# Performance work log

Measured on AMD Instinct MI355X. Metric: run time of the kernel, lower is better.

## Reference

```python
import jax, jax.numpy as jnp
import numpy as np

BLK = 128          # stk blocking
HID = 1024         # hidden_size
FFN = 4096         # ffn_hidden_size per expert
NE = 8             # moe_num_experts
TOK = 8192         # padded tokens (multiple of BLK)


def setup_inputs() -> dict:
    key = jax.random.key(0)
    k1, k2, k3 = jax.random.split(key, 3)
    x = jax.random.normal(k1, (TOK, HID), dtype=jnp.float32)
    w1 = jax.random.normal(k2, (NE * FFN, HID), dtype=jnp.float32) * 0.02
    n_row_blocks = TOK // BLK          # 64
    cols_per_expert = FFN // BLK       # 32
    # dMoE topology: each token row-block is assigned one expert; its nonzero
    # column blocks are all ffn blocks of that expert.
    expert_assign = jax.random.randint(k3, (n_row_blocks,), 0, NE)
    row_indices = jnp.repeat(jnp.arange(n_row_blocks), cols_per_expert)
    column_indices = (expert_assign[:, None] * cols_per_expert
                      + jnp.arange(cols_per_expert)[None, :]).reshape(-1)
    return {
        "x": x,
        "w1": w1,
        "row_indices": row_indices.astype(jnp.int32),     # [nnz]
        "column_indices": column_indices.astype(jnp.int32),  # [nnz]
        "block": BLK,
    }


def reference(x, w1, row_indices, column_indices, block):
    # sdd(x, w1.T, topo): out block k = x_block[row_indices[k]] @ w1_block[column_indices[k]].T
    hid = x.shape[1]
    xb = x.reshape(-1, block, hid)    # [n_row_blocks, blk, hid]
    wb = w1.reshape(-1, block, hid)   # [n_col_blocks, blk, hid]
    # [nnz, blk, blk] block-sparse data of the output matrix
    return jnp.einsum('kbh,kch->kbc', xb[row_indices], wb[column_indices])
```

## Files before the change

kernel.cpp:

```cpp
#include <hip/hip_runtime.h>
#include <hip/hip_bf16.h>
#include <stdint.h>

#define HID 1024
#define BLKDIM 128
#define BKT 32
#define NKT (HID / BKT)
#define NBUF 3

using short8 = __attribute__((ext_vector_type(8))) short;
using f32x4  = __attribute__((ext_vector_type(4))) float;
using f32x4v = __attribute__((ext_vector_type(4))) float;

__device__ __forceinline__ uint32_t bfround(float f) {
    uint32_t u = __builtin_bit_cast(uint32_t, f);
    return (u + 0x7FFFu + ((u >> 16) & 1u)) >> 16;
}

__device__ __forceinline__ void gld16(const ushort* g, const ushort* lds_base) {
    __builtin_amdgcn_global_load_lds(
        (const __attribute__((address_space(1))) void*)g,
        (__attribute__((address_space(3))) void*)lds_base, 16, 0, 0);
}

__global__ __launch_bounds__(256)
void cvt_sched_kernel(const float* __restrict__ x, const float* __restrict__ w1,
                      uint4* __restrict__ xb, uint4* __restrict__ wb,
                      int nx8, int nw8,
                      const int* __restrict__ cind, int* __restrict__ perm) {
    const int t = threadIdx.x;
    if (blockIdx.x == 0) {
        __shared__ int er[64], srb[64], goff[9];
        if (t < 64) er[t] = (cind[t * 32] >> 5) & 7;
        __syncthreads();
        if (t == 0) {
            int cnt[8], off[8];
            for (int e = 0; e < 8; ++e) cnt[e] = 0;
            for (int r = 0; r < 64; ++r) cnt[er[r]]++;
            goff[0] = 0;
            for (int e = 0; e < 8; ++e) { goff[e + 1] = goff[e] + cnt[e]; off[e] = goff[e]; }
            for (int r = 0; r < 64; ++r) srb[off[er[r]]++] = r;
        }
        __syncthreads();
        for (int g = t; g < 1024; g += 256) {
            int e = 0;
            while (g >= goff[e + 1] * 16) ++e;
            const int ne = goff[e + 1] - goff[e];
            const int local = g - goff[e] * 16;
            const int j = local / ne;
            const int idx = local - j * ne;
            perm[g] = srb[goff[e] + idx] * 16 + j;
        }
    }
    const int i = blockIdx.x * 256 + t;
    if (i < nx8) {
        const f32x4v* s = reinterpret_cast<const f32x4v*>(x) + (size_t)i * 2;
        f32x4v v0 = __builtin_nontemporal_load(s);
        f32x4v v1 = __builtin_nontemporal_load(s + 1);
        uint4 w;
        w.x = bfround(v0.x) | (bfround(v0.y) << 16);
        w.y = bfround(v0.z) | (bfround(v0.w) << 16);
        w.z = bfround(v1.x) | (bfround(v1.y) << 16);
        w.w = bfround(v1.z) | (bfround(v1.w) << 16);
        xb[i] = w;
    } else if (i < nx8 + nw8) {
        const int j = i - nx8;
        const f32x4v* s = reinterpret_cast<const f32x4v*>(w1) + (size_t)j * 2;
        f32x4v v0 = __builtin_nontemporal_load(s);
        f32x4v v1 = __builtin_nontemporal_load(s + 1);
        uint4 w;
        w.x = bfround(v0.x) | (bfround(v0.y) << 16);
        w.y = bfround(v0.z) | (bfround(v0.w) << 16);
        w.z = bfround(v1.x) | (bfround(v1.y) << 16);
        w.w = bfround(v1.z) | (bfround(v1.w) << 16);
        wb[j] = w;
    }
}

__global__ __launch_bounds__(512, 4)
void sdd_pipe2_kernel(const ushort* __restrict__ xb, const ushort* __restrict__ wb,
                      const int* __restrict__ rind, const int* __restrict__ cind,
                      const int* __restrict__ perm,
                      float* __restrict__ out) {
    __shared__ ushort lds[NBUF * BLKDIM * BKT + NBUF * 2 * BLKDIM * BKT];

    int g = blockIdx.x;
    const int nwg = gridDim.x;
    if ((nwg & 7) == 0) {
        const int cpx = nwg >> 3;
        g = (g & 7) * cpx + (g >> 3);
    }
    g = perm[g];
    const int k0 = g * 2;
    const int r  = rind[k0];

    const int t = threadIdx.x;
    const int w = t >> 6;
    const int l = t & 63;

    ushort* sAb = lds;
    ushort* sBb = lds + NBUF * BLKDIM * BKT;

    const int unx   = (l & 7) ^ ((l >> 3) & 7);
    const int rin16 = 2 * (l >> 3) + (unx >> 2);
    const int kofs  = (unx & 3) * 8;

    const ushort* agb = xb + (size_t)(r * BLKDIM + w * 16 + rin16) * HID + kofs;
    const int cblk = cind[k0 + (w >> 2)];
    const ushort* bgb = wb + (size_t)(cblk * BLKDIM + (w & 3) * 32 + rin16) * HID + kofs;

    const int wr   = (w >> 2) * 64;
    const int wcol = (w & 3) * 64;
    const int ps_l = (((l >> 4) + ((l & 1) << 2)) ^ ((l & 15) >> 1)) * 8;
    const int rhalf = (l & 15) >> 1;

    int aoff[4], boff[4];
#pragma unroll
    for (int m = 0; m < 4; ++m) aoff[m] = (wr / 2 + m * 8 + rhalf) * 64 + ps_l;
#pragma unroll
    for (int n = 0; n < 4; ++n) boff[n] = (wcol / 2 + n * 8 + rhalf) * 64 + ps_l;

    f32x4 acc[4][4];
#pragma unroll
    for (int m = 0; m < 4; ++m)
#pragma unroll
        for (int n = 0; n < 4; ++n)
            acc[m][n] = (f32x4){0.f, 0.f, 0.f, 0.f};

    auto stage = [&](int b, int kt) {
        gld16(agb + kt * BKT, &sAb[b * 4096 + w * 512]);
        gld16(bgb + kt * BKT,                      &sBb[b * 8192 + (2 * w) * 512]);
        gld16(bgb + (size_t)16 * HID + kt * BKT,   &sBb[b * 8192 + (2 * w + 1) * 512]);
    };

    stage(0, 0);
    stage(1, 1);
    asm volatile("s_waitcnt vmcnt(3)" ::: "memory");
    __builtin_amdgcn_s_barrier();
    __builtin_amdgcn_sched_barrier(0);

    for (int kt = 0; kt < NKT; ++kt) {
        const int cur = kt % 3;
        const int nxt = (kt + 2) % 3;
        const bool pre = (kt + 2) < NKT;
        const ushort* sa = &sAb[cur * 4096];
        const ushort* sb = &sBb[cur * 8192];

        short8 aF[4], bF[4];
#pragma unroll
        for (int m = 0; m < 4; ++m)
            aF[m] = *reinterpret_cast<const short8*>(&sa[aoff[m]]);
#pragma unroll
        for (int n = 0; n < 4; ++n)
            bF[n] = *reinterpret_cast<const short8*>(&sb[boff[n]]);
        if (pre) stage(nxt, kt + 2);
        __builtin_amdgcn_s_setprio(1);
#pragma unroll
        for (int m = 0; m < 4; ++m)
#pragma unroll
            for (int n = 0; n < 4; ++n)
                acc[m][n] = __builtin_amdgcn_mfma_f32_16x16x32_bf16(aF[m], bF[n], acc[m][n], 0, 0, 0);
        __builtin_amdgcn_s_setprio(0);

        if (pre) asm volatile("s_waitcnt vmcnt(3)" ::: "memory");
        else     asm volatile("s_waitcnt vmcnt(0)" ::: "memory");
        __builtin_amdgcn_s_barrier();
        __builtin_amdgcn_sched_barrier(0);
    }

    const int blk = (w & 3) >> 1;
    float* op = out + (size_t)(k0 + blk) * (BLKDIM * BLKDIM);
    const int colbase = (wcol & 64) ? 64 : 0;
    float* scr = reinterpret_cast<float*>(lds) + w * 1216;

#pragma unroll
    for (int m = 0; m < 4; ++m) {
#pragma unroll
        for (int n = 0; n < 4; ++n)
#pragma unroll
            for (int j = 0; j < 4; ++j)
                scr[((l >> 4) * 4 + j) * 76 + n * 16 + (l & 15)] = acc[m][n][j];
#pragma unroll
        for (int rg = 0; rg < 4; ++rg) {
            const int tr = rg * 4 + (l >> 4);
            f32x4 v = *reinterpret_cast<const f32x4*>(&scr[tr * 76 + (l & 15) * 4]);
            __builtin_nontemporal_store(v,
                reinterpret_cast<f32x4*>(&op[(size_t)(wr + m * 16 + tr) * BLKDIM
                                             + colbase + (l & 15) * 4]));
        }
    }
}

__device__ __forceinline__ void store16f(ushort* dst, float4 v0, float4 v1, float4 v2, float4 v3) {
    uint4 w0, w1;
    w0.x = bfround(v0.x) | (bfround(v0.y) << 16);
    w0.y = bfround(v0.z) | (bfround(v0.w) << 16);
    w0.z = bfround(v1.x) | (bfround(v1.y) << 16);
    w0.w = bfround(v1.z) | (bfround(v1.w) << 16);
    w1.x = bfround(v2.x) | (bfround(v2.y) << 16);
    w1.y = bfround(v2.z) | (bfround(v2.w) << 16);
    w1.z = bfround(v3.x) | (bfround(v3.y) << 16);
    w1.w = bfround(v3.z) | (bfround(v3.w) << 16);
    uint4* d = reinterpret_cast<uint4*>(dst);
    d[0] = w0; d[1] = w1;
}

__global__ __launch_bounds__(256, 2)
void sdd_bf16_kernel(const float* __restrict__ x, const float* __restrict__ w1,
                     const int* __restrict__ rind, const int* __restrict__ cind,
                     float* __restrict__ out) {
    __shared__ ushort sA[2][BLKDIM * 32];
    __shared__ ushort sB[2][BLKDIM * 32];
    const int k = blockIdx.x;
    const int t = threadIdx.x;
    const int r = rind[k];
    const int c = cind[k];
    const float* Abase = x  + (size_t)r * BLKDIM * HID;
    const float* Bbase = w1 + (size_t)c * BLKDIM * HID;
    const int srow = t >> 1, shalf = t & 1;
    const float* aptr = Abase + (size_t)srow * HID + shalf * 16;
    const float* bptr = Bbase + (size_t)srow * HID + shalf * 16;
    const int soff = srow * 32 + shalf * 16;
    const int wv = t >> 6, lane = t & 63;
    const int wr = (wv >> 1) * 64, wc = (wv & 1) * 64;
    const int lr = lane & 15, lk = (lane >> 4) * 8;
    f32x4 acc[4][4];
#pragma unroll
    for (int m = 0; m < 4; ++m)
#pragma unroll
        for (int n = 0; n < 4; ++n) acc[m][n] = (f32x4){0.f, 0.f, 0.f, 0.f};
    float4 ra[4], rb[4];
#pragma unroll
    for (int i = 0; i < 4; ++i) {
        ra[i] = *reinterpret_cast<const float4*>(aptr + i * 4);
        rb[i] = *reinterpret_cast<const float4*>(bptr + i * 4);
    }
    store16f(&sA[0][soff], ra[0], ra[1], ra[2], ra[3]);
    store16f(&sB[0][soff], rb[0], rb[1], rb[2], rb[3]);
    __syncthreads();
    for (int kt = 0; kt < 32; ++kt) {
        const int cur = kt & 1;
        if (kt + 1 < 32) {
            const float* ap = aptr + (kt + 1) * 32;
            const float* bp = bptr + (kt + 1) * 32;
#pragma unroll
            for (int i = 0; i < 4; ++i) {
                ra[i] = *reinterpret_cast<const float4*>(ap + i * 4);
                rb[i] = *reinterpret_cast<const float4*>(bp + i * 4);
            }
        }
        const ushort* sa = sA[cur];
        const ushort* sb = sB[cur];
        short8 aF[4], bF[4];
#pragma unroll
        for (int m = 0; m < 4; ++m) aF[m] = *reinterpret_cast<const short8*>(&sa[(wr + m * 16 + lr) * 32 + lk]);
#pragma unroll
        for (int n = 0; n < 4; ++n) bF[n] = *reinterpret_cast<const short8*>(&sb[(wc + n * 16 + lr) * 32 + lk]);
#pragma unroll
        for (int m = 0; m < 4; ++m)
#pragma unroll
            for (int n = 0; n < 4; ++n)
                acc[m][n] = __builtin_amdgcn_mfma_f32_16x16x32_bf16(aF[m], bF[n], acc[m][n], 0, 0, 0);
        if (kt + 1 < 32) {
            store16f(&sA[cur ^ 1][soff], ra[0], ra[1], ra[2], ra[3]);
            store16f(&sB[cur ^ 1][soff], rb[0], rb[1], rb[2], rb[3]);
        }
        __syncthreads();
    }
    float* op = out + (size_t)k * (BLKDIM * BLKDIM);
    const int rbase = wr + (lane >> 4) * 4;
#pragma unroll
    for (int m = 0; m < 4; ++m)
#pragma unroll
        for (int n = 0; n < 4; ++n) {
            const int col = wc + n * 16 + lr;
#pragma unroll
            for (int j = 0; j < 4; ++j)
                op[(size_t)(rbase + m * 16 + j) * BLKDIM + col] = acc[m][n][j];
        }
}

extern "C" void kernel_launch(void* const* d_in, const int* in_sizes, int n_in,
                              void* d_out, int out_size, void* d_ws, size_t ws_size,
                              hipStream_t stream) {
    const float* x  = (const float*)d_in[0];
    const float* w1 = (const float*)d_in[1];
    const int* ri   = (const int*)d_in[2];
    const int* ci   = (const int*)d_in[3];
    float* out      = (float*)d_out;
    const int nnz   = in_sizes[2];
    const int nx    = in_sizes[0];
    const int nw    = in_sizes[1];

    const size_t need = ((size_t)nx + (size_t)nw) * sizeof(ushort) + 4096 * sizeof(int);
    if (ws_size >= need && nnz == 2048 && nx == 8388608) {
        ushort* xb = (ushort*)d_ws;
        ushort* wb = xb + nx;
        int* perm  = (int*)(wb + nw);
        const int nx8 = nx / 8, nw8 = nw / 8;
        const int ncvt = (nx8 + nw8 + 255) / 256;
        hipLaunchKernelGGL(cvt_sched_kernel, dim3(ncvt), dim3(256), 0, stream,
                           x, w1, (uint4*)xb, (uint4*)wb, nx8, nw8, ci, perm);
        hipLaunchKernelGGL(sdd_pipe2_kernel, dim3(nnz / 2), dim3(512), 0, stream,
                           xb, wb, ri, ci, perm, out);
    } else {
        hipLaunchKernelGGL(sdd_bf16_kernel, dim3(nnz), dim3(256), 0, stream,
                           x, w1, ri, ci, out);
    }
}
```

Measured before the change: 125.7 us.

## Use 4 waves per workgroup with larger 64x128 per-wave tiles

The main GEMM kernel goes from 512 threads with 64x64 per-wave tiles to 256 threads where each wave computes a 64x128 tile (4x8 MFMA blocks). Each wave now issues six global-to-LDS loads per stage instead of three. Larger per-wave tiles raise MFMA work per LDS fragment read, but double the accumulator registers and lower occupancy to 2 workgroups per CU. The launch guard also now checks the weight size.

Measured after the change: 123.3 us, median of 2. No clear change (-1.9%).

```diff
diff --git a/kernel.cpp b/kernel.cpp
--- a/kernel.cpp
+++ b/kernel.cpp
@@ -77,11 +77,11 @@
     }
 }
 
-__global__ __launch_bounds__(512, 4)
-void sdd_pipe2_kernel(const ushort* __restrict__ xb, const ushort* __restrict__ wb,
-                      const int* __restrict__ rind, const int* __restrict__ cind,
-                      const int* __restrict__ perm,
-                      float* __restrict__ out) {
+__global__ __launch_bounds__(256, 2)
+void sdd_wide_kernel(const ushort* __restrict__ xb, const ushort* __restrict__ wb,
+                     const int* __restrict__ rind, const int* __restrict__ cind,
+                     const int* __restrict__ perm,
+                     float* __restrict__ out) {
     __shared__ ushort lds[NBUF * BLKDIM * BKT + NBUF * 2 * BLKDIM * BKT];
 
     int g = blockIdx.x;
@@ -105,37 +105,40 @@
     const int rin16 = 2 * (l >> 3) + (unx >> 2);
     const int kofs  = (unx & 3) * 8;
 
-    const ushort* agb = xb + (size_t)(r * BLKDIM + w * 16 + rin16) * HID + kofs;
-    const int cblk = cind[k0 + (w >> 2)];
-    const ushort* bgb = wb + (size_t)(cblk * BLKDIM + (w & 3) * 32 + rin16) * HID + kofs;
-
-    const int wr   = (w >> 2) * 64;
-    const int wcol = (w & 3) * 64;
+    const ushort* agb = xb + (size_t)(r * BLKDIM + w * 32 + rin16) * HID + kofs;
+    const int cblk = cind[k0 + (w >> 1)];
+    const ushort* bgb = wb + (size_t)(cblk * BLKDIM + (w & 1) * 64 + rin16) * HID + kofs;
+
+    const int wr   = (w >> 1) * 64;
+    const int wblk = w & 1;
     const int ps_l = (((l >> 4) + ((l & 1) << 2)) ^ ((l & 15) >> 1)) * 8;
     const int rhalf = (l & 15) >> 1;
 
-    int aoff[4], boff[4];
-#pragma unroll
-    for (int m = 0; m < 4; ++m) aoff[m] = (wr / 2 + m * 8 + rhalf) * 64 + ps_l;
-#pragma unroll
-    for (int n = 0; n < 4; ++n) boff[n] = (wcol / 2 + n * 8 + rhalf) * 64 + ps_l;
-
-    f32x4 acc[4][4];
+    int aoff[4], boff[8];
+#pragma unroll
+    for (int m = 0; m < 4; ++m) aoff[m] = ((w >> 1) * 32 + m * 8 + rhalf) * 64 + ps_l;
+#pragma unroll
+    for (int n = 0; n < 8; ++n) boff[n] = (wblk * 64 + n * 8 + rhalf) * 64 + ps_l;
+
+    f32x4 acc[4][8];
 #pragma unroll
     for (int m = 0; m < 4; ++m)
 #pragma unroll
-        for (int n = 0; n < 4; ++n)
+        for (int n = 0; n < 8; ++n)
             acc[m][n] = (f32x4){0.f, 0.f, 0.f, 0.f};
 
     auto stage = [&](int b, int kt) {
-        gld16(agb + kt * BKT, &sAb[b * 4096 + w * 512]);
-        gld16(bgb + kt * BKT,                      &sBb[b * 8192 + (2 * w) * 512]);
-        gld16(bgb + (size_t)16 * HID + kt * BKT,   &sBb[b * 8192 + (2 * w + 1) * 512]);
+        gld16(agb + kt * BKT,                          &sAb[b * 4096 + w * 1024]);
+        gld16(agb + (size_t)16 * HID + kt * BKT,       &sAb[b * 4096 + w * 1024 + 512]);
+        gld16(bgb + kt * BKT,                          &sBb[b * 8192 + w * 2048]);
+        gld16(bgb + (size_t)16 * HID + kt * BKT,       &sBb[b * 8192 + w * 2048 + 512]);
+        gld16(bgb + (size_t)32 * HID + kt * BKT,       &sBb[b * 8192 + w * 2048 + 1024]);
+        gld16(bgb + (size_t)48 * HID + kt * BKT,       &sBb[b * 8192 + w * 2048 + 1536]);
     };
 
     stage(0, 0);
     stage(1, 1);
-    asm volatile("s_waitcnt vmcnt(3)" ::: "memory");
+    asm volatile("s_waitcnt vmcnt(6)" ::: "memory");
     __builtin_amdgcn_s_barrier();
     __builtin_amdgcn_sched_barrier(0);
 
@@ -146,49 +149,49 @@
         const ushort* sa = &sAb[cur * 4096];
         const ushort* sb = &sBb[cur * 8192];
 
-        short8 aF[4], bF[4];
+        short8 aF[4], bF[8];
 #pragma unroll
         for (int m = 0; m < 4; ++m)
             aF[m] = *reinterpret_cast<const short8*>(&sa[aoff[m]]);
 #pragma unroll
-        for (int n = 0; n < 4; ++n)
+        for (int n = 0; n < 8; ++n)
             bF[n] = *reinterpret_cast<const short8*>(&sb[boff[n]]);
         if (pre) stage(nxt, kt + 2);
         __builtin_amdgcn_s_setprio(1);
 #pragma unroll
         for (int m = 0; m < 4; ++m)
 #pragma unroll
-            for (int n = 0; n < 4; ++n)
+            for (int n = 0; n < 8; ++n)
                 acc[m][n] = __builtin_amdgcn_mfma_f32_16x16x32_bf16(aF[m], bF[n], acc[m][n], 0, 0, 0);
         __builtin_amdgcn_s_setprio(0);
 
-        if (pre) asm volatile("s_waitcnt vmcnt(3)" ::: "memory");
+        if (pre) asm volatile("s_waitcnt vmcnt(6)" ::: "memory");
         else     asm volatile("s_waitcnt vmcnt(0)" ::: "memory");
         __builtin_amdgcn_s_barrier();
         __builtin_amdgcn_sched_barrier(0);
     }
 
-    const int blk = (w & 3) >> 1;
-    float* op = out + (size_t)(k0 + blk) * (BLKDIM * BLKDIM);
-    const int colbase = (wcol & 64) ? 64 : 0;
+    float* op = out + (size_t)(k0 + wblk) * (BLKDIM * BLKDIM);
     float* scr = reinterpret_cast<float*>(lds) + w * 1216;
 
 #pragma unroll
-    for (int m = 0; m < 4; ++m) {
-#pragma unroll
-        for (int n = 0; n < 4; ++n)
-#pragma unroll
-            for (int j = 0; j < 4; ++j)
-                scr[((l >> 4) * 4 + j) * 76 + n * 16 + (l & 15)] = acc[m][n][j];
-#pragma unroll
-        for (int rg = 0; rg < 4; ++rg) {
-            const int tr = rg * 4 + (l >> 4);
-            f32x4 v = *reinterpret_cast<const f32x4*>(&scr[tr * 76 + (l & 15) * 4]);
-            __builtin_nontemporal_store(v,
-                reinterpret_cast<f32x4*>(&op[(size_t)(wr + m * 16 + tr) * BLKDIM
-                                             + colbase + (l & 15) * 4]));
-        }
-    }
+    for (int m = 0; m < 4; ++m)
+#pragma unroll
+        for (int h = 0; h < 2; ++h) {
+#pragma unroll
+            for (int n = 0; n < 4; ++n)
+#pragma unroll
+                for (int j = 0; j < 4; ++j)
+                    scr[((l >> 4) * 4 + j) * 76 + n * 16 + (l & 15)] = acc[m][h * 4 + n][j];
+#pragma unroll
+            for (int rg = 0; rg < 4; ++rg) {
+                const int tr = rg * 4 + (l >> 4);
+                f32x4 v = *reinterpret_cast<const f32x4*>(&scr[tr * 76 + (l & 15) * 4]);
+                __builtin_nontemporal_store(v,
+                    reinterpret_cast<f32x4*>(&op[(size_t)(wr + m * 16 + tr) * BLKDIM
+                                                 + h * 64 + (l & 15) * 4]));
+            }
+        }
 }
 
 __device__ __forceinline__ void store16f(ushort* dst, float4 v0, float4 v1, float4 v2, float4 v3) {
@@ -293,7 +296,7 @@
     const int nw    = in_sizes[1];
 
     const size_t need = ((size_t)nx + (size_t)nw) * sizeof(ushort) + 4096 * sizeof(int);
-    if (ws_size >= need && nnz == 2048 && nx == 8388608) {
+    if (ws_size >= need && nnz == 2048 && nx == 8388608 && nw == 33554432) {
         ushort* xb = (ushort*)d_ws;
         ushort* wb = xb + nx;
         int* perm  = (int*)(wb + nw);
@@ -301,7 +304,7 @@
         const int ncvt = (nx8 + nw8 + 255) / 256;
         hipLaunchKernelGGL(cvt_sched_kernel, dim3(ncvt), dim3(256), 0, stream,
                            x, w1, (uint4*)xb, (uint4*)wb, nx8, nw8, ci, perm);
-        hipLaunchKernelGGL(sdd_pipe2_kernel, dim3(nnz / 2), dim3(512), 0, stream,
+        hipLaunchKernelGGL(sdd_wide_kernel, dim3(nnz / 2), dim3(256), 0, stream,
                            xb, wb, ri, ci, perm, out);
     } else {
         hipLaunchKernelGGL(sdd_bf16_kernel, dim3(nnz), dim3(256), 0, stream,
```
